# Optimization experiments

Hardware: AMD Instinct MI355X
Metric: run time of the kernel (lower is better)

## Reference

```python
import jax, jax.numpy as jnp
import numpy as np

MAX_LEVEL = 50

def _ln(x, g, b, eps=1e-5):
    m = jnp.mean(x, axis=-1, keepdims=True)
    v = jnp.mean((x - m) ** 2, axis=-1, keepdims=True)
    return (x - m) * jax.lax.rsqrt(v + eps) * g + b

def _mlp2(x, w1, b1, w2, b2):
    return jax.nn.relu(x @ w1 + b1) @ w2 + b2

def _forward(tokens, ln_g, ln_b, pw1, pb1, pw2, pb2, emb,
             sw1, sb1, sw2, sb2, ew1, eb1, ew2, eb2,
             spw1, spb1, spw2, spb2, lw1, lb1, lw2, lb2,
             fw, fb, fg, fbeta, aW, ab, ag, abt,
             dw1, db1, dw2, db2, levels, ph, pw):
    N = tokens.shape[0]
    f32 = tokens.dtype
    # token_norm + token_projection (Dropout is identity in eval)
    x = _ln(tokens, ln_g, ln_b)
    h = jax.nn.gelu(x @ pw1 + pb1, approximate=False) @ pw2 + pb2  # [N, D]
    idx = jnp.clip(levels[:, 0], 0, MAX_LEVEL)  # [N]
    h = h + emb[idx]
    # feature enhancement branch
    var = jnp.var(tokens, axis=-1, ddof=1, keepdims=True)            # torch.var unbiased
    mean = jnp.mean(tokens, axis=-1, keepdims=True)
    edge = jnp.mean(jnp.abs(jnp.diff(tokens, axis=-1)), axis=-1, keepdims=True)
    stats_feat = _mlp2(jnp.concatenate([var, mean], -1), sw1, sb1, sw2, sb2)
    spatial = jnp.broadcast_to(jnp.array([[ph, pw]], dtype=f32), (N, 2))
    spatial_feat = _mlp2(spatial, spw1, spb1, spw2, spb2)
    edge_feat = _mlp2(edge, ew1, eb1, ew2, eb2)
    lvl = jnp.broadcast_to(levels[0, 0].astype(f32)[None, None], (N, 1))
    level_feat = _mlp2(lvl, lw1, lb1, lw2, lb2)
    enh = jnp.concatenate([stats_feat, edge_feat, spatial_feat, level_feat], -1)  # [N, D]
    enh = jax.nn.gelu(_ln(enh @ fw + fb, fg, fbeta), approximate=False)
    h = h + 0.3 * enh
    # per-token scale adapter: MoE-style gather + tiny per-token GEMM + per-expert LN + GELU
    y = jnp.einsum('nd,ndf->nf', h, aW[idx]) + ab[idx]
    y = jax.nn.gelu(_ln(y, ag[idx], abt[idx]), approximate=False)
    # dynamic weighting gate
    w = jax.nn.sigmoid(_mlp2(y, dw1, db1, dw2, db2))  # [N, 1]
    return y * (0.8 + 0.4 * w)


def setup_inputs() -> dict:
    key = jax.random.key(0)
    ks = iter(jax.random.split(key, 64))
    def rn(shape, s=0.02):
        return jax.random.normal(next(ks), shape, dtype=jnp.float32) * s
    IN, D, D2, D4, DH, E, N = 768, 256, 512, 64, 128, 51, 4096
    return {
        'tokens': jax.random.normal(next(ks), (N, IN), dtype=jnp.float32),
        'ln_g': jnp.ones((IN,)), 'ln_b': jnp.zeros((IN,)),
        'pw1': rn((IN, D2)), 'pb1': jnp.zeros((D2,)),
        'pw2': rn((D2, D)), 'pb2': jnp.zeros((D,)),
        'emb': rn((E, D), 1.0),
        'sw1': rn((2, D4)), 'sb1': jnp.zeros((D4,)), 'sw2': rn((D4, D4)), 'sb2': jnp.zeros((D4,)),
        'ew1': rn((1, D4)), 'eb1': jnp.zeros((D4,)), 'ew2': rn((D4, D4)), 'eb2': jnp.zeros((D4,)),
        'spw1': rn((2, D4)), 'spb1': jnp.zeros((D4,)), 'spw2': rn((D4, D4)), 'spb2': jnp.zeros((D4,)),
        'lw1': rn((1, D4)), 'lb1': jnp.zeros((D4,)), 'lw2': rn((D4, D4)), 'lb2': jnp.zeros((D4,)),
        'fw': rn((D, D)), 'fb': jnp.zeros((D,)), 'fg': jnp.ones((D,)), 'fbeta': jnp.zeros((D,)),
        'aW': rn((E, D, D)), 'ab': jnp.zeros((E, D)), 'ag': jnp.ones((E, D)), 'abt': jnp.zeros((E, D)),
        'dw1': rn((D, DH)), 'db1': jnp.zeros((DH,)), 'dw2': rn((DH, 1)), 'db2': jnp.zeros((1,)),
        'levels': jax.random.randint(next(ks), (N, 2), 0, E),
        'ph': 4, 'pw': 4,
    }


def reference(tokens, ln_g, ln_b, pw1, pb1, pw2, pb2, emb,
              sw1, sb1, sw2, sb2, ew1, eb1, ew2, eb2,
              spw1, spb1, spw2, spb2, lw1, lb1, lw2, lb2,
              fw, fb, fg, fbeta, aW, ab, ag, abt,
              dw1, db1, dw2, db2, levels, ph, pw):
    return _forward(tokens, ln_g, ln_b, pw1, pb1, pw2, pb2, emb,
                    sw1, sb1, sw2, sb2, ew1, eb1, ew2, eb2,
                    spw1, spb1, spw2, spb2, lw1, lb1, lw2, lb2,
                    fw, fb, fg, fbeta, aW, ab, ag, abt,
                    dw1, db1, dw2, db2, levels, ph, pw)
```

## Files before the change

### kernel.cpp

```cpp
#include <hip/hip_runtime.h>
#include <math.h>

#define NTOK 4096
#define IND 768
#define DD 256
#define DD2 512
#define DHH 128
#define NEXP 51
#define TM 16
#define NTILE_MAX 312
#define NWCONV 968

typedef __attribute__((ext_vector_type(4))) float f32x4;
typedef __attribute__((ext_vector_type(8))) short short8;

__device__ __forceinline__ float gelu_f(float x) {
    return 0.5f * x * (1.0f + erff(x * 0.70710678118654752440f));
}
__device__ __forceinline__ ushort f2bf(float x) {
    unsigned u = __float_as_uint(x);
    return (ushort)((u + 0x7fffu + ((u >> 16) & 1u)) >> 16);
}
__device__ __forceinline__ void gl_lds16(const ushort* g, ushort* l) {
    __builtin_amdgcn_global_load_lds(
        (const __attribute__((address_space(1))) unsigned int*)g,
        (__attribute__((address_space(3))) unsigned int*)l, 16, 0, 0);
}

__global__ __launch_bounds__(256) void k_pre(
    const float* __restrict__ pw1, const float* __restrict__ pw2,
    const float* __restrict__ fw, const float* __restrict__ dw1,
    const float* __restrict__ aW,
    ushort* __restrict__ pw1T, ushort* __restrict__ pw2T, ushort* __restrict__ fwT,
    ushort* __restrict__ dw1T, ushort* __restrict__ aWT,
    const float* __restrict__ tokens,
    const float* __restrict__ ln_g, const float* __restrict__ ln_b,
    const float* __restrict__ sw1, const float* __restrict__ sb1,
    const float* __restrict__ sw2, const float* __restrict__ sb2,
    const float* __restrict__ ew1, const float* __restrict__ eb1,
    const float* __restrict__ ew2, const float* __restrict__ eb2,
    ushort* __restrict__ x_ln, ushort* __restrict__ enh,
    const int* __restrict__ levels,
    const float* __restrict__ spw1, const float* __restrict__ spb1,
    const float* __restrict__ spw2, const float* __restrict__ spb2,
    const float* __restrict__ lw1, const float* __restrict__ lb1,
    const float* __restrict__ lw2, const float* __restrict__ lb2,
    const int* __restrict__ ph, const int* __restrict__ pw,
    const float* __restrict__ fb,
    int* __restrict__ sorted, int* __restrict__ tpos, int* __restrict__ tcnt,
    int* __restrict__ texp, int* __restrict__ meta, float* __restrict__ ctail) {
    __shared__ float T[64][65];
    __shared__ int cnt[NEXP], cur[NEXP], offS[NEXP + 1], tileoff[NEXP + 1];
    __shared__ int expS[NTOK];
    __shared__ float hsS[64], hlS[64], cf[128];
    int t = threadIdx.x;

    if (blockIdx.x == 0) {
        if (t < NEXP) cnt[t] = 0;
        if (t < 64) {
            float p0 = (float)ph[0], p1 = (float)pw[0];
            float lvl = (float)levels[0];
            hsS[t] = fmaxf(0.f, p0 * spw1[t] + p1 * spw1[64 + t] + spb1[t]);
            hlS[t] = fmaxf(0.f, lvl * lw1[t] + lb1[t]);
        }
        __syncthreads();
        int myidx[16];
        #pragma unroll
        for (int i = 0; i < 16; ++i) {
            int n = t + i * 256;
            int id = min(max(levels[n * 2], 0), NEXP - 1);
            myidx[i] = id;
            atomicAdd(&cnt[id], 1);
        }
        if (t < 64) {
            float v = spb2[t];
            for (int j = 0; j < 64; ++j) v += hsS[j] * spw2[j * 64 + t];
            cf[t] = v;
        } else if (t < 128) {
            int k = t - 64;
            float v = lb2[k];
            for (int j = 0; j < 64; ++j) v += hlS[j] * lw2[j * 64 + k];
            cf[64 + k] = v;
        }
        __syncthreads();
        if (t == 0) {
            int a = 0, ta = 0;
            for (int e = 0; e < NEXP; ++e) {
                offS[e] = a; cur[e] = a; tileoff[e] = ta;
                ta += (cnt[e] + TM - 1) / TM;
                a += cnt[e];
            }
            offS[NEXP] = a; tileoff[NEXP] = ta;
            meta[0] = ta;
        }
        __syncthreads();
        #pragma unroll
        for (int i = 0; i < 16; ++i) {
            int n = t + i * 256;
            int p = atomicAdd(&cur[myidx[i]], 1);
            sorted[p] = n;
            expS[p] = myidx[i];
        }
        {
            float v = fb[t];
            for (int j = 0; j < 128; ++j) v += cf[j] * fw[(size_t)(128 + j) * DD + t];
            ctail[t] = v;
        }
        __syncthreads();
        #pragma unroll
        for (int i = 0; i < 16; ++i) {
            int p = t + i * 256;
            int e = expS[p];
            int rel = p - offS[e];
            if ((rel & (TM - 1)) == 0) {
                int ti = tileoff[e] + (rel / TM);
                tpos[ti] = p;
                tcnt[ti] = min(TM, offS[e + 1] - p);
                texp[ti] = e;
            }
        }
        return;
    }
    if (blockIdx.x < 1 + NWCONV) {
        int b = blockIdx.x - 1;
        const float* src; ushort* dst; int R, C;
        if (b < 96)       { src = pw1; dst = pw1T; R = IND; C = DD2; }
        else if (b < 128) { b -= 96;  src = pw2; dst = pw2T; R = DD2; C = DD; }
        else if (b < 144) { b -= 128; src = fw;  dst = fwT;  R = DD;  C = DD; }
        else if (b < 152) { b -= 144; src = dw1; dst = dw1T; R = DD;  C = DHH; }
        else { b -= 152; int e = b >> 4; b &= 15;
               src = aW + (size_t)e * DD * DD; dst = aWT + (size_t)e * DD * DD;
               R = DD; C = DD; }
        int tpc = C >> 6;
        int tr = b / tpc, tc = b - tr * tpc;
        int lr = t >> 6, lc = t & 63;
        #pragma unroll
        for (int i = 0; i < 16; ++i) {
            int r = i * 4 + lr;
            T[r][lc] = src[(size_t)(tr * 64 + r) * C + tc * 64 + lc];
        }
        __syncthreads();
        #pragma unroll
        for (int i = 0; i < 16; ++i) {
            int r = i * 4 + lr;
            dst[(size_t)(tc * 64 + r) * R + tr * 64 + lc] = f2bf(T[lc][r]);
        }
        return;
    }
    {
        int w = t >> 6, lane = t & 63;
        int n = (blockIdx.x - 1 - NWCONV) * 4 + w;
        const float* x = tokens + (size_t)n * IND;
        float v[12];
        {
            float4 va = *(const float4*)(x + lane * 12);
            float4 vb = *(const float4*)(x + lane * 12 + 4);
            float4 vc = *(const float4*)(x + lane * 12 + 8);
            v[0]=va.x; v[1]=va.y; v[2]=va.z; v[3]=va.w;
            v[4]=vb.x; v[5]=vb.y; v[6]=vb.z; v[7]=vb.w;
            v[8]=vc.x; v[9]=vc.y; v[10]=vc.z; v[11]=vc.w;
        }
        float s = 0.f, s2 = 0.f, es = 0.f;
        #pragma unroll
        for (int j = 0; j < 12; ++j) { s += v[j]; s2 += v[j] * v[j]; }
        float prev = __shfl_up(v[11], 1);
        if (lane > 0) es += fabsf(v[0] - prev);
        #pragma unroll
        for (int j = 1; j < 12; ++j) es += fabsf(v[j] - v[j - 1]);
        #pragma unroll
        for (int o = 1; o < 64; o <<= 1) {
            s  += __shfl_xor(s, o);
            s2 += __shfl_xor(s2, o);
            es += __shfl_xor(es, o);
        }
        float mean = s * (1.f / 768.f);
        float var_u = (s2 - 768.f * mean * mean) * (1.f / 767.f);
        float rstd = rsqrtf(s2 * (1.f / 768.f) - mean * mean + 1e-5f);
        float edge = es * (1.f / 767.f);
        ushort xl[12];
        #pragma unroll
        for (int j = 0; j < 12; ++j) {
            int e = lane * 12 + j;
            xl[j] = f2bf((v[j] - mean) * rstd * ln_g[e] + ln_b[e]);
        }
        ushort* xd = x_ln + (size_t)n * IND + lane * 12;
        *(ushort4*)(xd)     = *(ushort4*)&xl[0];
        *(ushort4*)(xd + 4) = *(ushort4*)&xl[4];
        *(ushort4*)(xd + 8) = *(ushort4*)&xl[8];
        float hs_ = fmaxf(0.f, var_u * sw1[lane] + mean * sw1[64 + lane] + sb1[lane]);
        float he_ = fmaxf(0.f, edge * ew1[lane] + eb1[lane]);
        float acc_s = sb2[lane], acc_e = eb2[lane];
        #pragma unroll 8
        for (int j = 0; j < 64; ++j) {
            float hj = __shfl(hs_, j);
            float ej = __shfl(he_, j);
            acc_s += hj * sw2[j * 64 + lane];
            acc_e += ej * ew2[j * 64 + lane];
        }
        ushort* er = enh + (size_t)n * DHH;
        er[lane] = f2bf(acc_s);
        er[64 + lane] = f2bf(acc_e);
    }
}

__global__ __launch_bounds__(512) void k_gemm1(
    const ushort* __restrict__ A, const ushort* __restrict__ BT,
    const float* __restrict__ bias, ushort* __restrict__ Cb) {
    const int N = DD2, K = IND;
    __shared__ ushort Al[128][64];
    __shared__ ushort Bl[64][64];
    int tid = threadIdx.x;
    int w = tid >> 6, lane = tid & 63;
    int g = lane >> 4, mr = lane & 15;
    int mq = w >> 1, nq = w & 1;
    int bm = blockIdx.y * 128, bn = blockIdx.x * 64;
    int r8 = lane >> 3, c = lane & 7, cg = c ^ r8;
    f32x4 acc[2][2];
    #pragma unroll
    for (int im = 0; im < 2; ++im)
        #pragma unroll
        for (int in = 0; in < 2; ++in) acc[im][in] = (f32x4){0.f, 0.f, 0.f, 0.f};
    for (int k0 = 0; k0 < K; k0 += 64) {
        #pragma unroll
        for (int i = 0; i < 2; ++i) {
            int r = 16 * w + 8 * i + r8;
            gl_lds16(A + (size_t)(bm + r) * K + k0 + cg * 8, &Al[16 * w + 8 * i][0]);
        }
        {
            int r = 8 * w + r8;
            gl_lds16(BT + (size_t)(bn + r) * K + k0 + cg * 8, &Bl[8 * w][0]);
        }
        asm volatile("s_waitcnt vmcnt(0)" ::: "memory");
        __syncthreads();
        #pragma unroll
        for (int kk = 0; kk < 64; kk += 32) {
            int jc = (kk >> 3) + g;
            int sw = ((jc ^ (mr & 7)) << 4);
            #pragma unroll
            for (int im = 0; im < 2; ++im) {
                short8 av = *(const short8*)((const char*)&Al[0][0] + (32 * mq + 16 * im + mr) * 128 + sw);
                #pragma unroll
                for (int in = 0; in < 2; ++in) {
                    short8 bv = *(const short8*)((const char*)&Bl[0][0] + (32 * nq + 16 * in + mr) * 128 + sw);
                    acc[im][in] = __builtin_amdgcn_mfma_f32_16x16x32_bf16(av, bv, acc[im][in], 0, 0, 0);
                }
            }
        }
        __syncthreads();
    }
    #pragma unroll
    for (int im = 0; im < 2; ++im) {
        #pragma unroll
        for (int in = 0; in < 2; ++in) {
            int col = bn + 32 * nq + 16 * in + mr;
            float bv = bias[col];
            #pragma unroll
            for (int r = 0; r < 4; ++r) {
                int row = bm + 32 * mq + 16 * im + 4 * g + r;
                Cb[(size_t)row * N + col] = f2bf(gelu_f(acc[im][in][r] + bv));
            }
        }
    }
}

__global__ __launch_bounds__(256) void k_mid(
    const ushort* __restrict__ h1, const ushort* __restrict__ pw2T,
    const float* __restrict__ pb2, const int* __restrict__ levels,
    const float* __restrict__ emb, float* __restrict__ h,
    const ushort* __restrict__ enh, const ushort* __restrict__ fwT,
    const float* __restrict__ ctail, float* __restrict__ e_pre) {
    __shared__ ushort Al[64][64];
    __shared__ ushort Bl[64][64];
    int by = blockIdx.y;
    const ushort* A; const ushort* BT; const float* bias; float* Cf;
    int K, sA, sB, epi, bm;
    if (by < 64) { A = h1; BT = pw2T; bias = pb2; Cf = h; K = DD2; sA = DD2; sB = DD2; epi = 2; bm = by * 64; }
    else         { A = enh; BT = fwT; bias = ctail; Cf = e_pre; K = DHH; sA = DHH; sB = DD; epi = 0; bm = (by - 64) * 64; }
    int tid = threadIdx.x;
    int w = tid >> 6, lane = tid & 63;
    int g = lane >> 4, mr = lane & 15;
    int bn = blockIdx.x * 64;
    int r8 = lane >> 3, c = lane & 7, cg = c ^ r8;
    f32x4 acc[4];
    #pragma unroll
    for (int f = 0; f < 4; ++f) acc[f] = (f32x4){0.f, 0.f, 0.f, 0.f};
    for (int k0 = 0; k0 < K; k0 += 64) {
        #pragma unroll
        for (int i = 0; i < 2; ++i) {
            int r = 16 * w + 8 * i + r8;
            gl_lds16(A + (size_t)(bm + r) * sA + k0 + cg * 8, &Al[16 * w + 8 * i][0]);
            gl_lds16(BT + (size_t)(bn + r) * sB + k0 + cg * 8, &Bl[16 * w + 8 * i][0]);
        }
        asm volatile("s_waitcnt vmcnt(0)" ::: "memory");
        __syncthreads();
        #pragma unroll
        for (int kk = 0; kk < 64; kk += 32) {
            int jc = (kk >> 3) + g;
            int sw = ((jc ^ (mr & 7)) << 4);
            short8 av = *(const short8*)((const char*)&Al[0][0] + (16 * w + mr) * 128 + sw);
            #pragma unroll
            for (int f = 0; f < 4; ++f) {
                short8 bv = *(const short8*)((const char*)&Bl[0][0] + (16 * f + mr) * 128 + sw);
                acc[f] = __builtin_amdgcn_mfma_f32_16x16x32_bf16(av, bv, acc[f], 0, 0, 0);
            }
        }
        __syncthreads();
    }
    #pragma unroll
    for (int f = 0; f < 4; ++f) {
        int col = bn + 16 * f + mr;
        float bv = bias[col];
        #pragma unroll
        for (int r = 0; r < 4; ++r) {
            int row = bm + 16 * w + 4 * g + r;
            float v = acc[f][r] + bv;
            if (epi == 2) {
                int id = min(max(levels[row * 2], 0), NEXP - 1);
                v += emb[(size_t)id * DD + col];
            }
            Cf[(size_t)row * DD + col] = v;
        }
    }
}

__global__ __launch_bounds__(256) void k_adapterF(
    const float* __restrict__ h, const float* __restrict__ e_pre,
    const float* __restrict__ fg, const float* __restrict__ fbeta,
    const ushort* __restrict__ aWT, const float* __restrict__ ab,
    const float* __restrict__ ag, const float* __restrict__ abt,
    const ushort* __restrict__ dw1T, const float* __restrict__ db1,
    const float* __restrict__ dw2, const float* __restrict__ db2,
    const int* __restrict__ sorted, const int* __restrict__ tpos,
    const int* __restrict__ tcnt, const int* __restrict__ texp,
    const int* __restrict__ meta, float* __restrict__ out) {
    __shared__ __align__(16) ushort Alf[TM][264];
    __shared__ __align__(16) ushort Bl[256][64];
    __shared__ __align__(16) ushort Dl[DHH][64];
    __shared__ int tokS[TM];
    __shared__ float gateS[TM];
    __shared__ float pg[4][TM];
    int b = blockIdx.x;
    if (b >= meta[0]) return;
    int tid = threadIdx.x, w = tid >> 6, lane = tid & 63;
    int g = lane >> 4, mr = lane & 15;
    int r8 = lane >> 3, c = lane & 7, cg = c ^ r8;
    int e = texp[b], base = tpos[b], nv = tcnt[b];
    if (tid < TM) tokS[tid] = sorted[base + min(tid, nv - 1)];
    __syncthreads();
    #pragma unroll
    for (int i = 0; i < 4; ++i) {
        int r = w * 4 + i;
        int tok = tokS[r];
        float4 e4 = *(const float4*)(e_pre + (size_t)tok * DD + lane * 4);
        float s = e4.x + e4.y + e4.z + e4.w;
        float s2 = e4.x * e4.x + e4.y * e4.y + e4.z * e4.z + e4.w * e4.w;
        #pragma unroll
        for (int o = 1; o < 64; o <<= 1) { s += __shfl_xor(s, o); s2 += __shfl_xor(s2, o); }
        float m = s * (1.f / 256.f);
        float rs = rsqrtf(s2 * (1.f / 256.f) - m * m + 1e-5f);
        float4 h4 = *(const float4*)(h + (size_t)tok * DD + lane * 4);
        float4 g4 = *(const float4*)(fg + lane * 4);
        float4 b4 = *(const float4*)(fbeta + lane * 4);
        ushort4 o4;
        o4.x = f2bf(h4.x + 0.3f * gelu_f((e4.x - m) * rs * g4.x + b4.x));
        o4.y = f2bf(h4.y + 0.3f * gelu_f((e4.y - m) * rs * g4.y + b4.y));
        o4.z = f2bf(h4.z + 0.3f * gelu_f((e4.z - m) * rs * g4.z + b4.z));
        o4.w = f2bf(h4.w + 0.3f * gelu_f((e4.w - m) * rs * g4.w + b4.w));
        *(ushort4*)&Alf[r][lane * 4] = o4;
    }
    __syncthreads();
    const ushort* We = aWT + (size_t)e * DD * DD;
    f32x4 acc[4];
    #pragma unroll
    for (int q = 0; q < 4; ++q) acc[q] = (f32x4){0.f, 0.f, 0.f, 0.f};
    for (int k0 = 0; k0 < DD; k0 += 64) {
        #pragma unroll
        for (int i = 0; i < 8; ++i) {
            int r = 64 * w + 8 * i + r8;
            gl_lds16(We + (size_t)r * DD + k0 + cg * 8, &Bl[64 * w + 8 * i][0]);
        }
        asm volatile("s_waitcnt vmcnt(0)" ::: "memory");
        __syncthreads();
        #pragma unroll
        for (int kk = 0; kk < 64; kk += 32) {
            int jc = (kk >> 3) + g;
            int sw = ((jc ^ (mr & 7)) << 4);
            short8 av = *(const short8*)&Alf[mr][k0 + kk + g * 8];
            #pragma unroll
            for (int q = 0; q < 4; ++q) {
                short8 bv = *(const short8*)((const char*)&Bl[0][0] + (64 * w + 16 * q + mr) * 128 + sw);
                acc[q] = __builtin_amdgcn_mfma_f32_16x16x32_bf16(av, bv, acc[q], 0, 0, 0);
            }
        }
        __syncthreads();
    }
    float* yf32 = (float*)&Bl[0][0];
    #pragma unroll
    for (int q = 0; q < 4; ++q) {
        int col = 64 * w + 16 * q + mr;
        float abv = ab[(size_t)e * DD + col];
        #pragma unroll
        for (int r = 0; r < 4; ++r) {
            int row = 4 * g + r;
            yf32[row * 260 + col] = acc[q][r] + abv;
        }
    }
    __syncthreads();
    #pragma unroll
    for (int i = 0; i < 4; ++i) {
        int r = w * 4 + i;
        float4 v = *(const float4*)&yf32[r * 260 + lane * 4];
        float s = v.x + v.y + v.z + v.w;
        float s2 = v.x * v.x + v.y * v.y + v.z * v.z + v.w * v.w;
        #pragma unroll
        for (int o = 1; o < 64; o <<= 1) { s += __shfl_xor(s, o); s2 += __shfl_xor(s2, o); }
        float m = s * (1.f / 256.f);
        float rs = rsqrtf(s2 * (1.f / 256.f) - m * m + 1e-5f);
        float4 gg = *(const float4*)(ag + (size_t)e * DD + lane * 4);
        float4 bb = *(const float4*)(abt + (size_t)e * DD + lane * 4);
        float4 y;
        y.x = gelu_f((v.x - m) * rs * gg.x + bb.x);
        y.y = gelu_f((v.y - m) * rs * gg.y + bb.y);
        y.z = gelu_f((v.z - m) * rs * gg.z + bb.z);
        y.w = gelu_f((v.w - m) * rs * gg.w + bb.w);
        *(float4*)&yf32[r * 260 + lane * 4] = y;
        ushort4 o4 = {f2bf(y.x), f2bf(y.y), f2bf(y.z), f2bf(y.w)};
        *(ushort4*)&Alf[r][lane * 4] = o4;
    }
    __syncthreads();
    f32x4 acc2[2];
    acc2[0] = (f32x4){0.f, 0.f, 0.f, 0.f};
    acc2[1] = (f32x4){0.f, 0.f, 0.f, 0.f};
    for (int k0 = 0; k0 < DD; k0 += 64) {
        #pragma unroll
        for (int i = 0; i < 4; ++i) {
            int r = 32 * w + 8 * i + r8;
            gl_lds16(dw1T + (size_t)r * DD + k0 + cg * 8, &Dl[32 * w + 8 * i][0]);
        }
        asm volatile("s_waitcnt vmcnt(0)" ::: "memory");
        __syncthreads();
        #pragma unroll
        for (int kk = 0; kk < 64; kk += 32) {
            int jc = (kk >> 3) + g;
            int sw = ((jc ^ (mr & 7)) << 4);
            short8 av = *(const short8*)&Alf[mr][k0 + kk + g * 8];
            #pragma unroll
            for (int q = 0; q < 2; ++q) {
                short8 bv = *(const short8*)((const char*)&Dl[0][0] + (32 * w + 16 * q + mr) * 128 + sw);
                acc2[q] = __builtin_amdgcn_mfma_f32_16x16x32_bf16(av, bv, acc2[q], 0, 0, 0);
            }
        }
        __syncthreads();
    }
    float pv[4] = {0.f, 0.f, 0.f, 0.f};
    #pragma unroll
    for (int q = 0; q < 2; ++q) {
        int col = 32 * w + 16 * q + mr;
        float d1 = db1[col], d2 = dw2[col];
        #pragma unroll
        for (int r = 0; r < 4; ++r)
            pv[r] += fmaxf(acc2[q][r] + d1, 0.f) * d2;
    }
    #pragma unroll
    for (int o = 1; o < 16; o <<= 1) {
        #pragma unroll
        for (int r = 0; r < 4; ++r) pv[r] += __shfl_xor(pv[r], o);
    }
    if (mr == 0) {
        #pragma unroll
        for (int r = 0; r < 4; ++r)
            pg[w][4 * g + r] = pv[r];
    }
    __syncthreads();
    if (tid < TM) {
        float p = pg[0][tid] + pg[1][tid] + pg[2][tid] + pg[3][tid] + db2[0];
        gateS[tid] = 0.8f + 0.4f / (1.f + expf(-p));
    }
    __syncthreads();
    {
        int row = tid >> 4, c0 = (tid & 15) * 16;
        if (row < nv) {
            int tok = tokS[row];
            float gt = gateS[row];
            #pragma unroll
            for (int j = 0; j < 4; ++j) {
                float4 v = *(const float4*)&yf32[row * 260 + c0 + j * 4];
                v.x *= gt; v.y *= gt; v.z *= gt; v.w *= gt;
                *(float4*)(out + (size_t)tok * DD + c0 + j * 4) = v;
            }
        }
    }
}

extern "C" void kernel_launch(void* const* d_in, const int* in_sizes, int n_in,
                              void* d_out, int out_size, void* d_ws, size_t ws_size,
                              hipStream_t stream) {
    const float* tokens = (const float*)d_in[0];
    const float* ln_g = (const float*)d_in[1];
    const float* ln_b = (const float*)d_in[2];
    const float* pw1 = (const float*)d_in[3];
    const float* pb1 = (const float*)d_in[4];
    const float* pw2 = (const float*)d_in[5];
    const float* pb2 = (const float*)d_in[6];
    const float* emb = (const float*)d_in[7];
    const float* sw1 = (const float*)d_in[8];
    const float* sb1 = (const float*)d_in[9];
    const float* sw2 = (const float*)d_in[10];
    const float* sb2 = (const float*)d_in[11];
    const float* ew1 = (const float*)d_in[12];
    const float* eb1 = (const float*)d_in[13];
    const float* ew2 = (const float*)d_in[14];
    const float* eb2 = (const float*)d_in[15];
    const float* spw1 = (const float*)d_in[16];
    const float* spb1 = (const float*)d_in[17];
    const float* spw2 = (const float*)d_in[18];
    const float* spb2 = (const float*)d_in[19];
    const float* lw1 = (const float*)d_in[20];
    const float* lb1 = (const float*)d_in[21];
    const float* lw2 = (const float*)d_in[22];
    const float* lb2 = (const float*)d_in[23];
    const float* fw = (const float*)d_in[24];
    const float* fb = (const float*)d_in[25];
    const float* fg = (const float*)d_in[26];
    const float* fbeta = (const float*)d_in[27];
    const float* aW = (const float*)d_in[28];
    const float* ab = (const float*)d_in[29];
    const float* ag = (const float*)d_in[30];
    const float* abt = (const float*)d_in[31];
    const float* dw1 = (const float*)d_in[32];
    const float* db1 = (const float*)d_in[33];
    const float* dw2 = (const float*)d_in[34];
    const float* db2 = (const float*)d_in[35];
    const int* levels = (const int*)d_in[36];
    const int* ph = (const int*)d_in[37];
    const int* pw = (const int*)d_in[38];
    float* outp = (float*)d_out;

    char* wsb = (char*)d_ws;
    ushort* x_ln  = (ushort*)wsb;  wsb += (size_t)NTOK * IND * 2;
    ushort* h1    = (ushort*)wsb;  wsb += (size_t)NTOK * DD2 * 2;
    ushort* enh   = (ushort*)wsb;  wsb += (size_t)NTOK * DHH * 2;
    float*  h     = (float*)wsb;   wsb += (size_t)NTOK * DD * 4;
    float*  e_pre = (float*)wsb;   wsb += (size_t)NTOK * DD * 4;
    ushort* pw1T  = (ushort*)wsb;  wsb += (size_t)DD2 * IND * 2;
    ushort* pw2T  = (ushort*)wsb;  wsb += (size_t)DD * DD2 * 2;
    ushort* fwT   = (ushort*)wsb;  wsb += (size_t)DD * DD * 2;
    ushort* aWT   = (ushort*)wsb;  wsb += (size_t)NEXP * DD * DD * 2;
    ushort* dw1T  = (ushort*)wsb;  wsb += (size_t)DHH * DD * 2;
    float*  ctail = (float*)wsb;   wsb += DD * 4;
    int*    sorted = (int*)wsb;    wsb += NTOK * 4;
    int*    tpos   = (int*)wsb;    wsb += NTILE_MAX * 4;
    int*    tcnt   = (int*)wsb;    wsb += NTILE_MAX * 4;
    int*    texp   = (int*)wsb;    wsb += NTILE_MAX * 4;
    int*    meta   = (int*)wsb;    wsb += 64;

    k_pre<<<1 + NWCONV + NTOK / 4, 256, 0, stream>>>(
        pw1, pw2, fw, dw1, aW, pw1T, pw2T, fwT, dw1T, aWT,
        tokens, ln_g, ln_b, sw1, sb1, sw2, sb2, ew1, eb1, ew2, eb2,
        x_ln, enh, levels,
        spw1, spb1, spw2, spb2, lw1, lb1, lw2, lb2, ph, pw, fb,
        sorted, tpos, tcnt, texp, meta, ctail);
    k_gemm1<<<dim3(DD2 / 64, NTOK / 128), 512, 0, stream>>>(x_ln, pw1T, pb1, h1);
    k_mid<<<dim3(DD / 64, 128), 256, 0, stream>>>(
        h1, pw2T, pb2, levels, emb, h, enh, fwT, ctail, e_pre);
    k_adapterF<<<NTILE_MAX, 256, 0, stream>>>(
        h, e_pre, fg, fbeta, aWT, ab, ag, abt, dw1T, db1, dw2, db2,
        sorted, tpos, tcnt, texp, meta, outp);
}
```

Measured before the change: 70.17 us.

## Fuse projection-out and enhancement GEMMs into per-expert adapter kernel

Removes the separate k_mid kernel and computes the pw2 projection (plus bias and level embedding) and the fw enhancement GEMM inside the adapter kernel, per 16-token tile gathered by expert. This drops the fp32 h and e_pre round-trips through global memory and one kernel launch. In exchange, each of up to 312 tiles reloads the full pw2T and fwT weights, at low MFMA utilisation from 16-row tiles. Shared memory is reorganised into reused buffers.

```diff
diff --git a/kernel.cpp b/kernel.cpp
--- a/kernel.cpp
+++ b/kernel.cpp
@@ -263,68 +263,11 @@
     }
 }
 
-__global__ __launch_bounds__(256) void k_mid(
-    const ushort* __restrict__ h1, const ushort* __restrict__ pw2T,
-    const float* __restrict__ pb2, const int* __restrict__ levels,
-    const float* __restrict__ emb, float* __restrict__ h,
-    const ushort* __restrict__ enh, const ushort* __restrict__ fwT,
-    const float* __restrict__ ctail, float* __restrict__ e_pre) {
-    __shared__ ushort Al[64][64];
-    __shared__ ushort Bl[64][64];
-    int by = blockIdx.y;
-    const ushort* A; const ushort* BT; const float* bias; float* Cf;
-    int K, sA, sB, epi, bm;
-    if (by < 64) { A = h1; BT = pw2T; bias = pb2; Cf = h; K = DD2; sA = DD2; sB = DD2; epi = 2; bm = by * 64; }
-    else         { A = enh; BT = fwT; bias = ctail; Cf = e_pre; K = DHH; sA = DHH; sB = DD; epi = 0; bm = (by - 64) * 64; }
-    int tid = threadIdx.x;
-    int w = tid >> 6, lane = tid & 63;
-    int g = lane >> 4, mr = lane & 15;
-    int bn = blockIdx.x * 64;
-    int r8 = lane >> 3, c = lane & 7, cg = c ^ r8;
-    f32x4 acc[4];
-    #pragma unroll
-    for (int f = 0; f < 4; ++f) acc[f] = (f32x4){0.f, 0.f, 0.f, 0.f};
-    for (int k0 = 0; k0 < K; k0 += 64) {
-        #pragma unroll
-        for (int i = 0; i < 2; ++i) {
-            int r = 16 * w + 8 * i + r8;
-            gl_lds16(A + (size_t)(bm + r) * sA + k0 + cg * 8, &Al[16 * w + 8 * i][0]);
-            gl_lds16(BT + (size_t)(bn + r) * sB + k0 + cg * 8, &Bl[16 * w + 8 * i][0]);
-        }
-        asm volatile("s_waitcnt vmcnt(0)" ::: "memory");
-        __syncthreads();
-        #pragma unroll
-        for (int kk = 0; kk < 64; kk += 32) {
-            int jc = (kk >> 3) + g;
-            int sw = ((jc ^ (mr & 7)) << 4);
-            short8 av = *(const short8*)((const char*)&Al[0][0] + (16 * w + mr) * 128 + sw);
-            #pragma unroll
-            for (int f = 0; f < 4; ++f) {
-                short8 bv = *(const short8*)((const char*)&Bl[0][0] + (16 * f + mr) * 128 + sw);
-                acc[f] = __builtin_amdgcn_mfma_f32_16x16x32_bf16(av, bv, acc[f], 0, 0, 0);
-            }
-        }
-        __syncthreads();
-    }
-    #pragma unroll
-    for (int f = 0; f < 4; ++f) {
-        int col = bn + 16 * f + mr;
-        float bv = bias[col];
-        #pragma unroll
-        for (int r = 0; r < 4; ++r) {
-            int row = bm + 16 * w + 4 * g + r;
-            float v = acc[f][r] + bv;
-            if (epi == 2) {
-                int id = min(max(levels[row * 2], 0), NEXP - 1);
-                v += emb[(size_t)id * DD + col];
-            }
-            Cf[(size_t)row * DD + col] = v;
-        }
-    }
-}
-
 __global__ __launch_bounds__(256) void k_adapterF(
-    const float* __restrict__ h, const float* __restrict__ e_pre,
+    const ushort* __restrict__ h1, const ushort* __restrict__ enh,
+    const ushort* __restrict__ pw2T, const float* __restrict__ pb2,
+    const float* __restrict__ emb,
+    const ushort* __restrict__ fwT, const float* __restrict__ ctail,
     const float* __restrict__ fg, const float* __restrict__ fbeta,
     const ushort* __restrict__ aWT, const float* __restrict__ ab,
     const float* __restrict__ ag, const float* __restrict__ abt,
@@ -333,12 +276,19 @@
     const int* __restrict__ sorted, const int* __restrict__ tpos,
     const int* __restrict__ tcnt, const int* __restrict__ texp,
     const int* __restrict__ meta, float* __restrict__ out) {
+    __shared__ __align__(16) char smA[16384];
+    __shared__ __align__(16) char smB[32768];
     __shared__ __align__(16) ushort Alf[TM][264];
-    __shared__ __align__(16) ushort Bl[256][64];
-    __shared__ __align__(16) ushort Dl[DHH][64];
+    __shared__ __align__(16) ushort EnhS[TM][128];
     __shared__ int tokS[TM];
+    __shared__ float redS[4][TM][2];
     __shared__ float gateS[TM];
     __shared__ float pg[4][TM];
+    ushort* H1p = (ushort*)smA;
+    ushort* Dlp = (ushort*)smA;
+    ushort* Blp = (ushort*)smB;
+    float* yf32 = (float*)smB;
+
     int b = blockIdx.x;
     if (b >= meta[0]) return;
     int tid = threadIdx.x, w = tid >> 6, lane = tid & 63;
@@ -347,62 +297,152 @@
     int e = texp[b], base = tpos[b], nv = tcnt[b];
     if (tid < TM) tokS[tid] = sorted[base + min(tid, nv - 1)];
     __syncthreads();
+
     #pragma unroll
     for (int i = 0; i < 4; ++i) {
-        int r = w * 4 + i;
+        int r = 4 * w + i;
         int tok = tokS[r];
-        float4 e4 = *(const float4*)(e_pre + (size_t)tok * DD + lane * 4);
-        float s = e4.x + e4.y + e4.z + e4.w;
-        float s2 = e4.x * e4.x + e4.y * e4.y + e4.z * e4.z + e4.w * e4.w;
-        #pragma unroll
-        for (int o = 1; o < 64; o <<= 1) { s += __shfl_xor(s, o); s2 += __shfl_xor(s2, o); }
-        float m = s * (1.f / 256.f);
-        float rs = rsqrtf(s2 * (1.f / 256.f) - m * m + 1e-5f);
-        float4 h4 = *(const float4*)(h + (size_t)tok * DD + lane * 4);
-        float4 g4 = *(const float4*)(fg + lane * 4);
-        float4 b4 = *(const float4*)(fbeta + lane * 4);
-        ushort4 o4;
-        o4.x = f2bf(h4.x + 0.3f * gelu_f((e4.x - m) * rs * g4.x + b4.x));
-        o4.y = f2bf(h4.y + 0.3f * gelu_f((e4.y - m) * rs * g4.y + b4.y));
-        o4.z = f2bf(h4.z + 0.3f * gelu_f((e4.z - m) * rs * g4.z + b4.z));
-        o4.w = f2bf(h4.w + 0.3f * gelu_f((e4.w - m) * rs * g4.w + b4.w));
-        *(ushort4*)&Alf[r][lane * 4] = o4;
-    }
-    __syncthreads();
-    const ushort* We = aWT + (size_t)e * DD * DD;
-    f32x4 acc[4];
-    #pragma unroll
-    for (int q = 0; q < 4; ++q) acc[q] = (f32x4){0.f, 0.f, 0.f, 0.f};
-    for (int k0 = 0; k0 < DD; k0 += 64) {
+        gl_lds16(h1 + (size_t)tok * DD2 + ((lane ^ (r & 7)) << 3), H1p + r * DD2);
+    }
+    {
+        int row = 4 * w + (lane >> 4);
+        int tok = tokS[row];
+        int ch = lane & 15;
+        gl_lds16(enh + (size_t)tok * DHH + ((ch ^ (row & 7)) << 3), &EnhS[4 * w][0]);
+    }
+    asm volatile("s_waitcnt vmcnt(0)" ::: "memory");
+    __syncthreads();
+
+    f32x4 hacc[4];
+    #pragma unroll
+    for (int q = 0; q < 4; ++q) hacc[q] = (f32x4){0.f, 0.f, 0.f, 0.f};
+    for (int k0 = 0; k0 < DD2; k0 += 64) {
         #pragma unroll
         for (int i = 0; i < 8; ++i) {
             int r = 64 * w + 8 * i + r8;
-            gl_lds16(We + (size_t)r * DD + k0 + cg * 8, &Bl[64 * w + 8 * i][0]);
+            gl_lds16(pw2T + (size_t)r * DD2 + k0 + cg * 8, Blp + (64 * w + 8 * i) * 64);
         }
         asm volatile("s_waitcnt vmcnt(0)" ::: "memory");
         __syncthreads();
         #pragma unroll
         for (int kk = 0; kk < 64; kk += 32) {
-            int jc = (kk >> 3) + g;
-            int sw = ((jc ^ (mr & 7)) << 4);
+            int jc = ((k0 + kk) >> 3) + g;
+            short8 av = *(const short8*)((const char*)H1p + mr * 1024 + ((jc ^ (mr & 7)) << 4));
+            int swb = (((kk >> 3) + g) ^ (mr & 7)) << 4;
+            #pragma unroll
+            for (int q = 0; q < 4; ++q) {
+                short8 bv = *(const short8*)((const char*)Blp + (64 * w + 16 * q + mr) * 128 + swb);
+                hacc[q] = __builtin_amdgcn_mfma_f32_16x16x32_bf16(av, bv, hacc[q], 0, 0, 0);
+            }
+        }
+        __syncthreads();
+    }
+    f32x4 eacc[4];
+    #pragma unroll
+    for (int q = 0; q < 4; ++q) eacc[q] = (f32x4){0.f, 0.f, 0.f, 0.f};
+    for (int k0 = 0; k0 < DHH; k0 += 64) {
+        #pragma unroll
+        for (int i = 0; i < 8; ++i) {
+            int r = 64 * w + 8 * i + r8;
+            gl_lds16(fwT + (size_t)r * DD + k0 + cg * 8, Blp + (64 * w + 8 * i) * 64);
+        }
+        asm volatile("s_waitcnt vmcnt(0)" ::: "memory");
+        __syncthreads();
+        #pragma unroll
+        for (int kk = 0; kk < 64; kk += 32) {
+            int jc = ((k0 + kk) >> 3) + g;
+            short8 av = *(const short8*)((const char*)&EnhS[0][0] + mr * 256 + ((jc ^ (mr & 7)) << 4));
+            int swb = (((kk >> 3) + g) ^ (mr & 7)) << 4;
+            #pragma unroll
+            for (int q = 0; q < 4; ++q) {
+                short8 bv = *(const short8*)((const char*)Blp + (64 * w + 16 * q + mr) * 128 + swb);
+                eacc[q] = __builtin_amdgcn_mfma_f32_16x16x32_bf16(av, bv, eacc[q], 0, 0, 0);
+            }
+        }
+        __syncthreads();
+    }
+    #pragma unroll
+    for (int q = 0; q < 4; ++q) {
+        int col = 64 * w + 16 * q + mr;
+        float hb = pb2[col] + emb[(size_t)e * DD + col];
+        float cb2 = ctail[col];
+        #pragma unroll
+        for (int r4 = 0; r4 < 4; ++r4) {
+            hacc[q][r4] += hb;
+            eacc[q][r4] += cb2;
+        }
+    }
+    {
+        float s[4], s2[4];
+        #pragma unroll
+        for (int r4 = 0; r4 < 4; ++r4) {
+            s[r4] = eacc[0][r4] + eacc[1][r4] + eacc[2][r4] + eacc[3][r4];
+            s2[r4] = eacc[0][r4]*eacc[0][r4] + eacc[1][r4]*eacc[1][r4]
+                   + eacc[2][r4]*eacc[2][r4] + eacc[3][r4]*eacc[3][r4];
+        }
+        #pragma unroll
+        for (int o = 1; o < 16; o <<= 1) {
+            #pragma unroll
+            for (int r4 = 0; r4 < 4; ++r4) {
+                s[r4]  += __shfl_xor(s[r4], o);
+                s2[r4] += __shfl_xor(s2[r4], o);
+            }
+        }
+        if (mr == 0) {
+            #pragma unroll
+            for (int r4 = 0; r4 < 4; ++r4) {
+                redS[w][4 * g + r4][0] = s[r4];
+                redS[w][4 * g + r4][1] = s2[r4];
+            }
+        }
+    }
+    __syncthreads();
+    #pragma unroll
+    for (int r4 = 0; r4 < 4; ++r4) {
+        int row = 4 * g + r4;
+        float S  = redS[0][row][0] + redS[1][row][0] + redS[2][row][0] + redS[3][row][0];
+        float S2 = redS[0][row][1] + redS[1][row][1] + redS[2][row][1] + redS[3][row][1];
+        float m = S * (1.f / 256.f);
+        float rs = rsqrtf(S2 * (1.f / 256.f) - m * m + 1e-5f);
+        #pragma unroll
+        for (int q = 0; q < 4; ++q) {
+            int col = 64 * w + 16 * q + mr;
+            float enhv = gelu_f((eacc[q][r4] - m) * rs * fg[col] + fbeta[col]);
+            Alf[row][col] = f2bf(hacc[q][r4] + 0.3f * enhv);
+        }
+    }
+    __syncthreads();
+    const ushort* We = aWT + (size_t)e * DD * DD;
+    f32x4 yacc[4];
+    #pragma unroll
+    for (int q = 0; q < 4; ++q) yacc[q] = (f32x4){0.f, 0.f, 0.f, 0.f};
+    for (int k0 = 0; k0 < DD; k0 += 64) {
+        #pragma unroll
+        for (int i = 0; i < 8; ++i) {
+            int r = 64 * w + 8 * i + r8;
+            gl_lds16(We + (size_t)r * DD + k0 + cg * 8, Blp + (64 * w + 8 * i) * 64);
+        }
+        asm volatile("s_waitcnt vmcnt(0)" ::: "memory");
+        __syncthreads();
+        #pragma unroll
+        for (int kk = 0; kk < 64; kk += 32) {
             short8 av = *(const short8*)&Alf[mr][k0 + kk + g * 8];
+            int swb = (((kk >> 3) + g) ^ (mr & 7)) << 4;
             #pragma unroll
             for (int q = 0; q < 4; ++q) {
-                short8 bv = *(const short8*)((const char*)&Bl[0][0] + (64 * w + 16 * q + mr) * 128 + sw);
-                acc[q] = __builtin_amdgcn_mfma_f32_16x16x32_bf16(av, bv, acc[q], 0, 0, 0);
-            }
-        }
-        __syncthreads();
-    }
-    float* yf32 = (float*)&Bl[0][0];
+                short8 bv = *(const short8*)((const char*)Blp + (64 * w + 16 * q + mr) * 128 + swb);
+                yacc[q] = __builtin_amdgcn_mfma_f32_16x16x32_bf16(av, bv, yacc[q], 0, 0, 0);
+            }
+        }
+        __syncthreads();
+    }
     #pragma unroll
     for (int q = 0; q < 4; ++q) {
         int col = 64 * w + 16 * q + mr;
         float abv = ab[(size_t)e * DD + col];
         #pragma unroll
-        for (int r = 0; r < 4; ++r) {
-            int row = 4 * g + r;
-            yf32[row * 260 + col] = acc[q][r] + abv;
+        for (int r4 = 0; r4 < 4; ++r4) {
+            yf32[(4 * g + r4) * 260 + col] = yacc[q][r4] + abv;
         }
     }
     __syncthreads();
@@ -435,18 +475,17 @@
         #pragma unroll
         for (int i = 0; i < 4; ++i) {
             int r = 32 * w + 8 * i + r8;
-            gl_lds16(dw1T + (size_t)r * DD + k0 + cg * 8, &Dl[32 * w + 8 * i][0]);
+            gl_lds16(dw1T + (size_t)r * DD + k0 + cg * 8, Dlp + (32 * w + 8 * i) * 64);
         }
         asm volatile("s_waitcnt vmcnt(0)" ::: "memory");
         __syncthreads();
         #pragma unroll
         for (int kk = 0; kk < 64; kk += 32) {
-            int jc = (kk >> 3) + g;
-            int sw = ((jc ^ (mr & 7)) << 4);
             short8 av = *(const short8*)&Alf[mr][k0 + kk + g * 8];
+            int swb = (((kk >> 3) + g) ^ (mr & 7)) << 4;
             #pragma unroll
             for (int q = 0; q < 2; ++q) {
-                short8 bv = *(const short8*)((const char*)&Dl[0][0] + (32 * w + 16 * q + mr) * 128 + sw);
+                short8 bv = *(const short8*)((const char*)Dlp + (32 * w + 16 * q + mr) * 128 + swb);
                 acc2[q] = __builtin_amdgcn_mfma_f32_16x16x32_bf16(av, bv, acc2[q], 0, 0, 0);
             }
         }
@@ -458,18 +497,18 @@
         int col = 32 * w + 16 * q + mr;
         float d1 = db1[col], d2 = dw2[col];
         #pragma unroll
-        for (int r = 0; r < 4; ++r)
-            pv[r] += fmaxf(acc2[q][r] + d1, 0.f) * d2;
+        for (int r4 = 0; r4 < 4; ++r4)
+            pv[r4] += fmaxf(acc2[q][r4] + d1, 0.f) * d2;
     }
     #pragma unroll
     for (int o = 1; o < 16; o <<= 1) {
         #pragma unroll
-        for (int r = 0; r < 4; ++r) pv[r] += __shfl_xor(pv[r], o);
+        for (int r4 = 0; r4 < 4; ++r4) pv[r4] += __shfl_xor(pv[r4], o);
     }
     if (mr == 0) {
         #pragma unroll
-        for (int r = 0; r < 4; ++r)
-            pg[w][4 * g + r] = pv[r];
+        for (int r4 = 0; r4 < 4; ++r4)
+            pg[w][4 * g + r4] = pv[r4];
     }
     __syncthreads();
     if (tid < TM) {
@@ -540,8 +579,6 @@
     ushort* x_ln  = (ushort*)wsb;  wsb += (size_t)NTOK * IND * 2;
     ushort* h1    = (ushort*)wsb;  wsb += (size_t)NTOK * DD2 * 2;
     ushort* enh   = (ushort*)wsb;  wsb += (size_t)NTOK * DHH * 2;
-    float*  h     = (float*)wsb;   wsb += (size_t)NTOK * DD * 4;
-    float*  e_pre = (float*)wsb;   wsb += (size_t)NTOK * DD * 4;
     ushort* pw1T  = (ushort*)wsb;  wsb += (size_t)DD2 * IND * 2;
     ushort* pw2T  = (ushort*)wsb;  wsb += (size_t)DD * DD2 * 2;
     ushort* fwT   = (ushort*)wsb;  wsb += (size_t)DD * DD * 2;
@@ -561,9 +598,8 @@
         spw1, spb1, spw2, spb2, lw1, lb1, lw2, lb2, ph, pw, fb,
         sorted, tpos, tcnt, texp, meta, ctail);
     k_gemm1<<<dim3(DD2 / 64, NTOK / 128), 512, 0, stream>>>(x_ln, pw1T, pb1, h1);
-    k_mid<<<dim3(DD / 64, 128), 256, 0, stream>>>(
-        h1, pw2T, pb2, levels, emb, h, enh, fwT, ctail, e_pre);
     k_adapterF<<<NTILE_MAX, 256, 0, stream>>>(
-        h, e_pre, fg, fbeta, aWT, ab, ag, abt, dw1T, db1, dw2, db2,
+        h1, enh, pw2T, pb2, emb, fwT, ctail, fg, fbeta,
+        aWT, ab, ag, abt, dw1T, db1, dw2, db2,
         sorted, tpos, tcnt, texp, meta, outp);
 }
```

Result: faster. 64.51 us (-8.1%).
